# Optimization experiments

Measured on AMD Instinct MI355X. Metric: run time of the kernel, lower is better.

Reference implementation:

```python
import jax, jax.numpy as jnp
import numpy as np

TAU = 2.0        # spikingjelly LIFNode default tau
VTH = 1.0        # v_threshold
ALPHA = 2.0      # ATan surrogate alpha
NUM_HEADS = 8
N_WIN = 8
TOPK = 4


@jax.custom_vjp
def atan_heaviside(x):
    # spike = H(v - v_th), with ATan surrogate gradient
    return (x >= 0.0).astype(x.dtype)

def _ah_fwd(x):
    return atan_heaviside(x), x

def _ah_bwd(x, g):
    half_pi_alpha = np.float32(np.pi / 2.0 * ALPHA)
    return (g * (ALPHA / 2.0) / (1.0 + (half_pi_alpha * x) ** 2),)

atan_heaviside.defvjp(_ah_fwd, _ah_bwd)


def lif(x):
    """Multi-step LIF over leading time dim. decay_input=True, v_reset=0, detach_reset."""
    def step(v, xt):
        v = v + (xt - v) / TAU                      # charge
        s = atan_heaviside(v - VTH)                 # fire
        v = v * (1.0 - jax.lax.stop_gradient(s))    # hard reset (detached)
        return v, s
    _, spikes = jax.lax.scan(step, jnp.zeros_like(x[0]), x)
    return spikes


def setup_inputs() -> dict:
    key = jax.random.key(0)
    k1, k2, k3, k4, k5 = jax.random.split(key, 5)
    T, B, L, C = 4, 4, 1024, 256
    x = jax.random.normal(k1, (T, B, L, C), dtype=jnp.float32)
    w_qkv = jax.random.normal(k2, (C, 3 * C), dtype=jnp.float32) * (C ** -0.5)
    b_qkv = jax.random.normal(k3, (3 * C,), dtype=jnp.float32) * 0.02
    w_proj = jax.random.normal(k4, (C, C), dtype=jnp.float32) * (C ** -0.5)
    b_proj = jax.random.normal(k5, (C,), dtype=jnp.float32) * 0.02
    return {"x": x, "w_qkv": w_qkv, "b_qkv": b_qkv, "w_proj": w_proj, "b_proj": b_proj}


def reference(x, w_qkv, b_qkv, w_proj, b_proj):
    T, B, L, C = x.shape
    hd = C // NUM_HEADS
    win = L // N_WIN
    scale = hd ** -0.5

    # --- region-level routing (on raw input summed over time) ---
    xs = x.sum(axis=0).reshape(B, N_WIN, win, C)
    region = xs.sum(axis=2)                                  # [B, n_win, C]
    attn_r = jnp.einsum('bnc,bmc->bnm', region, region) * (C ** -0.5)
    _, idx = jax.lax.top_k(attn_r, TOPK)                     # [B, n_win, topk] int32

    # --- qkv + LIF spiking ---
    qkv = x @ w_qkv + b_qkv                                  # [T,B,L,3C]
    q, k, v = jnp.split(qkv, 3, axis=-1)
    q, k, v = lif(q), lif(k), lif(v)
    q = q.reshape(T, B, N_WIN, win, NUM_HEADS, hd)
    k = k.reshape(T, B, N_WIN, win, NUM_HEADS, hd)
    v = v.reshape(T, B, N_WIN, win, NUM_HEADS, hd)

    # --- gather routed KV windows (vectorized; topk-major concat like torch.cat) ---
    b_idx = jnp.arange(B)[:, None, None]                     # [B,1,1]
    k_g = k[:, b_idx, idx].reshape(T, B, N_WIN, TOPK * win, NUM_HEADS, hd)
    v_g = v[:, b_idx, idx].reshape(T, B, N_WIN, TOPK * win, NUM_HEADS, hd)

    # --- windowed attention over gathered keys ---
    attn = jnp.einsum('tbnqhd,tbnkhd->tbnhqk', q, k_g) * scale
    attn = jax.nn.softmax(attn, axis=-1)
    out = jnp.einsum('tbnhqk,tbnkhd->tbnqhd', attn, v_g).reshape(T, B, L, C)

    out = lif(out @ w_proj + b_proj)
    return out
```

## Files before the change

kernel.cpp:

```cpp
#include <hip/hip_runtime.h>
#include <cstdint>
#include <cstddef>

#define TT 4
#define BB 4
#define LL 1024
#define CC 256
#define HH 8
#define HD 32
#define NWIN 8
#define WIN 128
#define TOPKN 4
#define C3 768

__global__ __launch_bounds__(256) void region_kernel(const float* __restrict__ x,
                                                     float* __restrict__ region) {
    int bn = blockIdx.x;
    int b = bn >> 3, n = bn & 7;
    int c = threadIdx.x;
    float tot = 0.0f;
    for (int r = 0; r < WIN; ++r) {
        int l = n * WIN + r;
        float s = 0.0f;
        for (int t = 0; t < TT; ++t) {
            s += x[(((size_t)t * BB + b) * LL + l) * CC + c];
        }
        tot += s;
    }
    region[(size_t)bn * CC + c] = tot;
}

__global__ __launch_bounds__(64) void route_kernel(const float* __restrict__ region,
                                                   int* __restrict__ idx) {
    int b = blockIdx.x;
    __shared__ float reg[NWIN][CC];
    __shared__ float attn_r[NWIN][NWIN];
    int tid = threadIdx.x;
    for (int e = tid; e < NWIN * CC; e += 64)
        reg[e >> 8][e & 255] = region[(size_t)b * NWIN * CC + e];
    __syncthreads();
    int n = tid >> 3, m = tid & 7;
    float s = 0.0f;
    for (int c = 0; c < CC; ++c) s += reg[n][c] * reg[m][c];
    attn_r[n][m] = s * 0.0625f;
    __syncthreads();
    if (tid < NWIN) {
        float vals[NWIN];
        for (int m2 = 0; m2 < NWIN; ++m2) vals[m2] = attn_r[tid][m2];
        for (int kk = 0; kk < TOPKN; ++kk) {
            int bi = 0; float bv = vals[0];
            for (int m2 = 1; m2 < NWIN; ++m2) {
                if (vals[m2] > bv) { bv = vals[m2]; bi = m2; }
            }
            idx[(b * NWIN + tid) * TOPKN + kk] = bi;
            vals[bi] = -INFINITY;
        }
    }
}

__global__ __launch_bounds__(256, 2) void gemm_bias(const float* __restrict__ A,
                                                    const float* __restrict__ W,
                                                    const float* __restrict__ bias,
                                                    float* __restrict__ C,
                                                    int M, int N, int K) {
    const int BM = 128, BN = 128, BK = 16, TM = 8, TN = 8;
    __shared__ float As[BK][BM + 4];
    __shared__ float Bs[BK][BN];
    int tid = threadIdx.x;
    int tx = tid & 15, ty = tid >> 4;
    int bm = blockIdx.x * BM, bn = blockIdx.y * BN;
    float acc[TM][TN] = {};
    for (int k0 = 0; k0 < K; k0 += BK) {
#pragma unroll
        for (int it = 0; it < 2; ++it) {
            int i = it * 256 + tid;
            int row = i >> 2, kc = (i & 3) * 4;
            float4 v = *(const float4*)(A + (size_t)(bm + row) * K + k0 + kc);
            As[kc + 0][row] = v.x; As[kc + 1][row] = v.y;
            As[kc + 2][row] = v.z; As[kc + 3][row] = v.w;
        }
#pragma unroll
        for (int it = 0; it < 2; ++it) {
            int i = it * 256 + tid;
            int kr = i >> 5, nc = (i & 31) * 4;
            float4 v = *(const float4*)(W + (size_t)(k0 + kr) * N + bn + nc);
            *(float4*)&Bs[kr][nc] = v;
        }
        __syncthreads();
#pragma unroll
        for (int kk = 0; kk < BK; ++kk) {
            float a[TM], bb[TN];
            const float4* ap = (const float4*)&As[kk][ty * TM];
            float4 a0 = ap[0], a1 = ap[1];
            a[0]=a0.x; a[1]=a0.y; a[2]=a0.z; a[3]=a0.w;
            a[4]=a1.x; a[5]=a1.y; a[6]=a1.z; a[7]=a1.w;
            const float4* bp = (const float4*)&Bs[kk][tx * TN];
            float4 b0 = bp[0], b1 = bp[1];
            bb[0]=b0.x; bb[1]=b0.y; bb[2]=b0.z; bb[3]=b0.w;
            bb[4]=b1.x; bb[5]=b1.y; bb[6]=b1.z; bb[7]=b1.w;
#pragma unroll
            for (int i = 0; i < TM; ++i)
#pragma unroll
                for (int j = 0; j < TN; ++j)
                    acc[i][j] = fmaf(a[i], bb[j], acc[i][j]);
        }
        __syncthreads();
    }
#pragma unroll
    for (int i = 0; i < TM; ++i) {
        int row = bm + ty * TM + i;
        int col = bn + tx * TN;
        float4 o0 = make_float4(acc[i][0] + bias[col + 0], acc[i][1] + bias[col + 1],
                                acc[i][2] + bias[col + 2], acc[i][3] + bias[col + 3]);
        float4 o1 = make_float4(acc[i][4] + bias[col + 4], acc[i][5] + bias[col + 5],
                                acc[i][6] + bias[col + 6], acc[i][7] + bias[col + 7]);
        *(float4*)&C[(size_t)row * N + col]     = o0;
        *(float4*)&C[(size_t)row * N + col + 4] = o1;
    }
}

__global__ __launch_bounds__(256) void lif_kernel(const float* src, float* dst, size_t stride) {
    size_t i = ((size_t)blockIdx.x * blockDim.x + threadIdx.x) * 4;
    float v[4] = {0.f, 0.f, 0.f, 0.f};
    for (int t = 0; t < TT; ++t) {
        float4 xv4 = *(const float4*)(src + (size_t)t * stride + i);
        float xv[4] = {xv4.x, xv4.y, xv4.z, xv4.w};
        float sp[4];
#pragma unroll
        for (int j = 0; j < 4; ++j) {
            v[j] = v[j] + (xv[j] - v[j]) * 0.5f;
            bool fire = (v[j] >= 1.0f);
            sp[j] = fire ? 1.0f : 0.0f;
            v[j] = fire ? 0.0f : v[j];
        }
        *(float4*)(dst + (size_t)t * stride + i) = make_float4(sp[0], sp[1], sp[2], sp[3]);
    }
}

__global__ __launch_bounds__(256) void pack_kernel(const float* __restrict__ spk,
                                                   uint32_t* __restrict__ pk) {
    size_t g = (size_t)blockIdx.x * 256 + threadIdx.x;
    int row = (int)(g >> 9);
    int col = (int)(g & 511);
    float v = spk[(size_t)row * C3 + col];
    unsigned long long m = __ballot(v >= 0.5f);
    int lane = threadIdx.x & 63;
    if ((lane & 31) == 0)
        pk[(size_t)row * 16 + (col >> 5)] = (lane < 32) ? (uint32_t)m : (uint32_t)(m >> 32);
}

__global__ __launch_bounds__(256) void attn_sm(const uint32_t* __restrict__ pk,
                                               const int* __restrict__ idxws,
                                               float2* __restrict__ amz) {
    int bid = blockIdx.x;
    int hp = bid & 3, n = (bid >> 2) & 7, b = (bid >> 5) & 3, t = bid >> 7;
    __shared__ uint32_t kbs[2][512];
    int tid = threadIdx.x;
    int q = tid & 127, h = tid >> 7;
    int lbase = (t * BB + b) * LL;

    const int* ip = idxws + (b * NWIN + n) * TOPKN;
    int s0r = ip[0], s1r = ip[1], s2r = ip[2], s3r = ip[3];

#pragma unroll 4
    for (int e = tid; e < 1024; e += 256) {
        int hh = e >> 9, kk = e & 511;
        int w = kk >> 7;
        int sw = (w == 0) ? s0r : (w == 1) ? s1r : (w == 2) ? s2r : s3r;
        int row = sw * WIN + (kk & 127);
        kbs[hh][kk] = pk[(size_t)(lbase + row) * 16 + 8 + hp * 2 + hh];
    }
    uint32_t qw = pk[(size_t)(lbase + n * WIN + q) * 16 + hp * 2 + h];
    __syncthreads();

    const float ALPHA_SC = 0.17677669529663687f;
    const uint4* kb4 = (const uint4*)kbs[h];
    int smax = 0;
#pragma unroll 8
    for (int k4 = 0; k4 < 128; ++k4) {
        uint4 w4 = kb4[k4];
        smax = max(smax, __popc(qw & w4.x));
        smax = max(smax, __popc(qw & w4.y));
        smax = max(smax, __popc(qw & w4.z));
        smax = max(smax, __popc(qw & w4.w));
    }
    float am = __fmul_rn((float)smax, ALPHA_SC);
    float Z = 0.0f;
#pragma unroll 4
    for (int k4 = 0; k4 < 128; ++k4) {
        uint4 w4 = kb4[k4];
        Z += expf(__fsub_rn(__fmul_rn((float)__popc(qw & w4.x), ALPHA_SC), am));
        Z += expf(__fsub_rn(__fmul_rn((float)__popc(qw & w4.y), ALPHA_SC), am));
        Z += expf(__fsub_rn(__fmul_rn((float)__popc(qw & w4.z), ALPHA_SC), am));
        Z += expf(__fsub_rn(__fmul_rn((float)__popc(qw & w4.w), ALPHA_SC), am));
    }
    amz[(size_t)(lbase + n * WIN + q) * HH + hp * 2 + h] = make_float2(am, Z);
}

__global__ __launch_bounds__(128, 2) void attn_pv(const float* __restrict__ spk,
                                                  const uint32_t* __restrict__ pk,
                                                  const int* __restrict__ idxws,
                                                  const float2* __restrict__ amz,
                                                  float* __restrict__ out) {
    int bid = blockIdx.x;
    int h = bid & 1, hp = (bid >> 1) & 3, n = (bid >> 3) & 7, b = (bid >> 6) & 3, t = bid >> 8;
    __shared__ __align__(16) float Vlds[2][64][32];
    __shared__ float    ptab[33][WIN];
    __shared__ uint32_t kbs[4 * WIN];
    int tid = threadIdx.x;
    int qg = tid & 63, dh = tid >> 6;
    int lbase = (t * BB + b) * LL;

    const int* ip = idxws + (b * NWIN + n) * TOPKN;
    int sidx[TOPKN];
    sidx[0] = ip[0]; sidx[1] = ip[1]; sidx[2] = ip[2]; sidx[3] = ip[3];

#pragma unroll 4
    for (int e = tid; e < 512; e += 128) {
        int w = e >> 7;
        int sw = sidx[w];
        int row = sw * WIN + (e & 127);
        kbs[e] = pk[(size_t)(lbase + row) * 16 + 8 + hp * 2 + h];
    }
    uint32_t qw0 = pk[(size_t)(lbase + n * WIN + qg) * 16 + hp * 2 + h];
    uint32_t qw1 = pk[(size_t)(lbase + n * WIN + qg + 64) * 16 + hp * 2 + h];

    {
        float2 az = amz[(size_t)(lbase + n * WIN + tid) * HH + hp * 2 + h];
        const float ALPHA_SC = 0.17677669529663687f;
        for (int s = 0; s <= 32; ++s)
            ptab[s][tid] = expf(__fsub_rn(__fmul_rn((float)s, ALPHA_SC), az.x)) / az.y;
    }

    const float* vsrc = spk + (size_t)lbase * C3 + 512 + hp * 64 + h * 32
                        + (size_t)(tid >> 3) * C3 + (tid & 7) * 4;
    int wvoff = (tid >> 6) * 1024;

#define STAGE_HALF(hw_)                                                              \
    do {                                                                             \
        int hw = (hw_);                                                              \
        const float* src = vsrc + (size_t)sidx[hw >> 1] * (WIN * C3)                 \
                                + (size_t)(hw & 1) * 64 * C3;                        \
        char* lbasep = (char*)(&Vlds[hw & 1][0][0]) + wvoff;                         \
        _Pragma("unroll")                                                            \
        for (int it = 0; it < 4; ++it) {                                             \
            __builtin_amdgcn_global_load_lds(                                        \
                (const __attribute__((address_space(1))) void*)(src + (size_t)it * 16 * C3), \
                (__attribute__((address_space(3))) void*)(lbasep + it * 2048),       \
                16, 0, 0);                                                           \
        }                                                                            \
    } while (0)

    STAGE_HALF(0);

    float acc0[16], acc1[16];
#pragma unroll
    for (int d = 0; d < 16; ++d) { acc0[d] = 0.0f; acc1[d] = 0.0f; }

    asm volatile("s_waitcnt vmcnt(0)" ::: "memory");
    __syncthreads();

    const uint4* kb4 = (const uint4*)kbs;

#pragma unroll
    for (int hw = 0; hw < 8; ++hw) {
        if (hw < 7) STAGE_HALF(hw + 1);

        const uint4* kw4 = kb4 + hw * 16;
        const float* pr = &Vlds[hw & 1][0][dh * 16];
#pragma unroll 4
        for (int g = 0; g < 16; ++g) {
            uint4 kw = kw4[g];
#pragma unroll
            for (int j = 0; j < 4; ++j) {
                uint32_t kwj = (j == 0) ? kw.x : (j == 1) ? kw.y : (j == 2) ? kw.z : kw.w;
                float P0 = ptab[__popc(qw0 & kwj)][qg];
                float P1 = ptab[__popc(qw1 & kwj)][qg + 64];
                const float4* vp = (const float4*)(pr + j * 32);
                float4 v0 = vp[0], v1 = vp[1], v2 = vp[2], v3 = vp[3];
                acc0[ 0] = fmaf(P0, v0.x, acc0[ 0]);  acc1[ 0] = fmaf(P1, v0.x, acc1[ 0]);
                acc0[ 1] = fmaf(P0, v0.y, acc0[ 1]);  acc1[ 1] = fmaf(P1, v0.y, acc1[ 1]);
                acc0[ 2] = fmaf(P0, v0.z, acc0[ 2]);  acc1[ 2] = fmaf(P1, v0.z, acc1[ 2]);
                acc0[ 3] = fmaf(P0, v0.w, acc0[ 3]);  acc1[ 3] = fmaf(P1, v0.w, acc1[ 3]);
                acc0[ 4] = fmaf(P0, v1.x, acc0[ 4]);  acc1[ 4] = fmaf(P1, v1.x, acc1[ 4]);
                acc0[ 5] = fmaf(P0, v1.y, acc0[ 5]);  acc1[ 5] = fmaf(P1, v1.y, acc1[ 5]);
                acc0[ 6] = fmaf(P0, v1.z, acc0[ 6]);  acc1[ 6] = fmaf(P1, v1.z, acc1[ 6]);
                acc0[ 7] = fmaf(P0, v1.w, acc0[ 7]);  acc1[ 7] = fmaf(P1, v1.w, acc1[ 7]);
                acc0[ 8] = fmaf(P0, v2.x, acc0[ 8]);  acc1[ 8] = fmaf(P1, v2.x, acc1[ 8]);
                acc0[ 9] = fmaf(P0, v2.y, acc0[ 9]);  acc1[ 9] = fmaf(P1, v2.y, acc1[ 9]);
                acc0[10] = fmaf(P0, v2.z, acc0[10]);  acc1[10] = fmaf(P1, v2.z, acc1[10]);
                acc0[11] = fmaf(P0, v2.w, acc0[11]);  acc1[11] = fmaf(P1, v2.w, acc1[11]);
                acc0[12] = fmaf(P0, v3.x, acc0[12]);  acc1[12] = fmaf(P1, v3.x, acc1[12]);
                acc0[13] = fmaf(P0, v3.y, acc0[13]);  acc1[13] = fmaf(P1, v3.y, acc1[13]);
                acc0[14] = fmaf(P0, v3.z, acc0[14]);  acc1[14] = fmaf(P1, v3.z, acc1[14]);
                acc0[15] = fmaf(P0, v3.w, acc0[15]);  acc1[15] = fmaf(P1, v3.w, acc1[15]);
            }
            pr += 128;
        }

        asm volatile("s_waitcnt vmcnt(0)" ::: "memory");
        __syncthreads();
    }
#undef STAGE_HALF

    size_t ob0 = (size_t)(lbase + n * WIN + qg) * CC + (hp * 2 + h) * 32 + dh * 16;
    size_t ob1 = ob0 + (size_t)64 * CC;
#pragma unroll
    for (int d = 0; d < 16; ++d) out[ob0 + d] = acc0[d];
#pragma unroll
    for (int d = 0; d < 16; ++d) out[ob1 + d] = acc1[d];
}

extern "C" void kernel_launch(void* const* d_in, const int* in_sizes, int n_in,
                              void* d_out, int out_size, void* d_ws, size_t ws_size,
                              hipStream_t stream) {
    const float* x      = (const float*)d_in[0];
    const float* w_qkv  = (const float*)d_in[1];
    const float* b_qkv  = (const float*)d_in[2];
    const float* w_proj = (const float*)d_in[3];
    const float* b_proj = (const float*)d_in[4];
    float* ws = (float*)d_ws;

    float* qkv      = ws;
    float* attn_out = ws + 12582912;
    float* proj     = ws + 16777216;
    uint32_t* pkb   = (uint32_t*)proj;
    float* region   = ws + 20971520;
    int*   idxp     = (int*)(ws + 20979712);
    float2* amzp    = (float2*)(ws + 20979840);
    float* outp     = (float*)d_out;

    region_kernel<<<dim3(BB * NWIN), dim3(256), 0, stream>>>(x, region);
    route_kernel<<<dim3(BB), dim3(64), 0, stream>>>(region, idxp);
    gemm_bias<<<dim3(128, 6), dim3(256), 0, stream>>>(x, w_qkv, b_qkv, qkv,
                                                      TT * BB * LL, C3, CC);
    lif_kernel<<<dim3(3072), dim3(256), 0, stream>>>(qkv, qkv, (size_t)BB * LL * C3);
    pack_kernel<<<dim3(32768), dim3(256), 0, stream>>>(qkv, pkb);
    attn_sm<<<dim3(TT * BB * NWIN * 4), dim3(256), 0, stream>>>(pkb, idxp, amzp);
    attn_pv<<<dim3(TT * BB * NWIN * 4 * 2), dim3(128), 0, stream>>>(qkv, pkb, idxp, amzp, attn_out);
    gemm_bias<<<dim3(128, 2), dim3(256), 0, stream>>>(attn_out, w_proj, b_proj, proj,
                                                      TT * BB * LL, CC, CC);
    lif_kernel<<<dim3(1024), dim3(256), 0, stream>>>(proj, outp, (size_t)BB * LL * CC);
}
```

Measured before the change: 286.5 us.

## Fuse softmax stats into attention kernel, retile GEMMs, deepen V prefetch

Merges the separate softmax-statistics kernel into the PV attention kernel, so each block computes row max and normalizer from the packed spike bits in LDS and no longer round-trips them through global memory. The V staging becomes a two-deep prefetch with partial vmcnt waits so loads overlap with compute. The QKV GEMM changes its B-tile column mapping to split each thread's columns into two strided halves with padded LDS and raises its occupancy hint. The projection GEMM switches to a 64x64 tile kernel for more blocks. The fused kernel repeats the popcount max/sum work per block pair, and the extra staging adds LDS pressure.

```diff
diff --git a/kernel.cpp b/kernel.cpp
--- a/kernel.cpp
+++ b/kernel.cpp
@@ -58,18 +58,18 @@
     }
 }
 
-__global__ __launch_bounds__(256, 2) void gemm_bias(const float* __restrict__ A,
-                                                    const float* __restrict__ W,
-                                                    const float* __restrict__ bias,
-                                                    float* __restrict__ C,
-                                                    int M, int N, int K) {
-    const int BM = 128, BN = 128, BK = 16, TM = 8, TN = 8;
+__global__ __launch_bounds__(256, 3) void gemm_bias128(const float* __restrict__ A,
+                                                       const float* __restrict__ W,
+                                                       const float* __restrict__ bias,
+                                                       float* __restrict__ C,
+                                                       int M, int N, int K) {
+    const int BM = 128, BN = 128, BK = 16, TM = 8;
     __shared__ float As[BK][BM + 4];
-    __shared__ float Bs[BK][BN];
+    __shared__ float Bs[BK][136];
     int tid = threadIdx.x;
     int tx = tid & 15, ty = tid >> 4;
     int bm = blockIdx.x * BM, bn = blockIdx.y * BN;
-    float acc[TM][TN] = {};
+    float acc[TM][8] = {};
     for (int k0 = 0; k0 < K; k0 += BK) {
 #pragma unroll
         for (int it = 0; it < 2; ++it) {
@@ -89,19 +89,19 @@
         __syncthreads();
 #pragma unroll
         for (int kk = 0; kk < BK; ++kk) {
-            float a[TM], bb[TN];
+            float a[TM], bb[8];
             const float4* ap = (const float4*)&As[kk][ty * TM];
             float4 a0 = ap[0], a1 = ap[1];
             a[0]=a0.x; a[1]=a0.y; a[2]=a0.z; a[3]=a0.w;
             a[4]=a1.x; a[5]=a1.y; a[6]=a1.z; a[7]=a1.w;
-            const float4* bp = (const float4*)&Bs[kk][tx * TN];
-            float4 b0 = bp[0], b1 = bp[1];
+            float4 b0 = *(const float4*)&Bs[kk][tx * 4];
+            float4 b1 = *(const float4*)&Bs[kk][64 + tx * 4];
             bb[0]=b0.x; bb[1]=b0.y; bb[2]=b0.z; bb[3]=b0.w;
             bb[4]=b1.x; bb[5]=b1.y; bb[6]=b1.z; bb[7]=b1.w;
 #pragma unroll
             for (int i = 0; i < TM; ++i)
 #pragma unroll
-                for (int j = 0; j < TN; ++j)
+                for (int j = 0; j < 8; ++j)
                     acc[i][j] = fmaf(a[i], bb[j], acc[i][j]);
         }
         __syncthreads();
@@ -109,13 +109,63 @@
 #pragma unroll
     for (int i = 0; i < TM; ++i) {
         int row = bm + ty * TM + i;
-        int col = bn + tx * TN;
-        float4 o0 = make_float4(acc[i][0] + bias[col + 0], acc[i][1] + bias[col + 1],
-                                acc[i][2] + bias[col + 2], acc[i][3] + bias[col + 3]);
-        float4 o1 = make_float4(acc[i][4] + bias[col + 4], acc[i][5] + bias[col + 5],
-                                acc[i][6] + bias[col + 6], acc[i][7] + bias[col + 7]);
-        *(float4*)&C[(size_t)row * N + col]     = o0;
-        *(float4*)&C[(size_t)row * N + col + 4] = o1;
+        int col0 = bn + tx * 4;
+        int col1 = bn + 64 + tx * 4;
+        float4 o0 = make_float4(acc[i][0] + bias[col0 + 0], acc[i][1] + bias[col0 + 1],
+                                acc[i][2] + bias[col0 + 2], acc[i][3] + bias[col0 + 3]);
+        float4 o1 = make_float4(acc[i][4] + bias[col1 + 0], acc[i][5] + bias[col1 + 1],
+                                acc[i][6] + bias[col1 + 2], acc[i][7] + bias[col1 + 3]);
+        *(float4*)&C[(size_t)row * N + col0] = o0;
+        *(float4*)&C[(size_t)row * N + col1] = o1;
+    }
+}
+
+__global__ __launch_bounds__(256, 4) void gemm_bias64(const float* __restrict__ A,
+                                                      const float* __restrict__ W,
+                                                      const float* __restrict__ bias,
+                                                      float* __restrict__ C,
+                                                      int M, int N, int K) {
+    const int BM = 64, BN = 64, BK = 16;
+    __shared__ float As[BK][BM + 4];
+    __shared__ float Bs[BK][72];
+    int tid = threadIdx.x;
+    int tx = tid & 15, ty = tid >> 4;
+    int bm = blockIdx.x * BM, bn = blockIdx.y * BN;
+    float acc[4][4] = {};
+    for (int k0 = 0; k0 < K; k0 += BK) {
+        {
+            int row = tid >> 2, kc = (tid & 3) * 4;
+            float4 v = *(const float4*)(A + (size_t)(bm + row) * K + k0 + kc);
+            As[kc + 0][row] = v.x; As[kc + 1][row] = v.y;
+            As[kc + 2][row] = v.z; As[kc + 3][row] = v.w;
+        }
+        {
+            int kr = tid >> 4, nc = (tid & 15) * 4;
+            float4 v = *(const float4*)(W + (size_t)(k0 + kr) * N + bn + nc);
+            *(float4*)&Bs[kr][nc] = v;
+        }
+        __syncthreads();
+#pragma unroll
+        for (int kk = 0; kk < BK; ++kk) {
+            float4 av = *(const float4*)&As[kk][ty * 4];
+            float4 bv = *(const float4*)&Bs[kk][tx * 4];
+            float a[4] = {av.x, av.y, av.z, av.w};
+            float bb[4] = {bv.x, bv.y, bv.z, bv.w};
+#pragma unroll
+            for (int i = 0; i < 4; ++i)
+#pragma unroll
+                for (int j = 0; j < 4; ++j)
+                    acc[i][j] = fmaf(a[i], bb[j], acc[i][j]);
+        }
+        __syncthreads();
+    }
+#pragma unroll
+    for (int i = 0; i < 4; ++i) {
+        int row = bm + ty * 4 + i;
+        int col = bn + tx * 4;
+        float4 o = make_float4(acc[i][0] + bias[col + 0], acc[i][1] + bias[col + 1],
+                               acc[i][2] + bias[col + 2], acc[i][3] + bias[col + 3]);
+        *(float4*)&C[(size_t)row * N + col] = o;
     }
 }
 
@@ -149,64 +199,15 @@
         pk[(size_t)row * 16 + (col >> 5)] = (lane < 32) ? (uint32_t)m : (uint32_t)(m >> 32);
 }
 
-__global__ __launch_bounds__(256) void attn_sm(const uint32_t* __restrict__ pk,
-                                               const int* __restrict__ idxws,
-                                               float2* __restrict__ amz) {
-    int bid = blockIdx.x;
-    int hp = bid & 3, n = (bid >> 2) & 7, b = (bid >> 5) & 3, t = bid >> 7;
-    __shared__ uint32_t kbs[2][512];
-    int tid = threadIdx.x;
-    int q = tid & 127, h = tid >> 7;
-    int lbase = (t * BB + b) * LL;
-
-    const int* ip = idxws + (b * NWIN + n) * TOPKN;
-    int s0r = ip[0], s1r = ip[1], s2r = ip[2], s3r = ip[3];
-
-#pragma unroll 4
-    for (int e = tid; e < 1024; e += 256) {
-        int hh = e >> 9, kk = e & 511;
-        int w = kk >> 7;
-        int sw = (w == 0) ? s0r : (w == 1) ? s1r : (w == 2) ? s2r : s3r;
-        int row = sw * WIN + (kk & 127);
-        kbs[hh][kk] = pk[(size_t)(lbase + row) * 16 + 8 + hp * 2 + hh];
-    }
-    uint32_t qw = pk[(size_t)(lbase + n * WIN + q) * 16 + hp * 2 + h];
-    __syncthreads();
-
-    const float ALPHA_SC = 0.17677669529663687f;
-    const uint4* kb4 = (const uint4*)kbs[h];
-    int smax = 0;
-#pragma unroll 8
-    for (int k4 = 0; k4 < 128; ++k4) {
-        uint4 w4 = kb4[k4];
-        smax = max(smax, __popc(qw & w4.x));
-        smax = max(smax, __popc(qw & w4.y));
-        smax = max(smax, __popc(qw & w4.z));
-        smax = max(smax, __popc(qw & w4.w));
-    }
-    float am = __fmul_rn((float)smax, ALPHA_SC);
-    float Z = 0.0f;
-#pragma unroll 4
-    for (int k4 = 0; k4 < 128; ++k4) {
-        uint4 w4 = kb4[k4];
-        Z += expf(__fsub_rn(__fmul_rn((float)__popc(qw & w4.x), ALPHA_SC), am));
-        Z += expf(__fsub_rn(__fmul_rn((float)__popc(qw & w4.y), ALPHA_SC), am));
-        Z += expf(__fsub_rn(__fmul_rn((float)__popc(qw & w4.z), ALPHA_SC), am));
-        Z += expf(__fsub_rn(__fmul_rn((float)__popc(qw & w4.w), ALPHA_SC), am));
-    }
-    amz[(size_t)(lbase + n * WIN + q) * HH + hp * 2 + h] = make_float2(am, Z);
-}
-
-__global__ __launch_bounds__(128, 2) void attn_pv(const float* __restrict__ spk,
-                                                  const uint32_t* __restrict__ pk,
-                                                  const int* __restrict__ idxws,
-                                                  const float2* __restrict__ amz,
-                                                  float* __restrict__ out) {
+__global__ __launch_bounds__(128, 2) void attn_fused(const float* __restrict__ spk,
+                                                     const uint32_t* __restrict__ pk,
+                                                     const int* __restrict__ idxws,
+                                                     float* __restrict__ out) {
     int bid = blockIdx.x;
     int h = bid & 1, hp = (bid >> 1) & 3, n = (bid >> 3) & 7, b = (bid >> 6) & 3, t = bid >> 8;
     __shared__ __align__(16) float Vlds[2][64][32];
-    __shared__ float    ptab[33][WIN];
-    __shared__ uint32_t kbs[4 * WIN];
+    __shared__ float ptab[33][WIN];
+    __shared__ __align__(16) uint32_t kbs[4 * WIN];
     int tid = threadIdx.x;
     int qg = tid & 63, dh = tid >> 6;
     int lbase = (t * BB + b) * LL;
@@ -218,19 +219,13 @@
 #pragma unroll 4
     for (int e = tid; e < 512; e += 128) {
         int w = e >> 7;
-        int sw = sidx[w];
-        int row = sw * WIN + (e & 127);
+        int row = sidx[w] * WIN + (e & 127);
         kbs[e] = pk[(size_t)(lbase + row) * 16 + 8 + hp * 2 + h];
     }
     uint32_t qw0 = pk[(size_t)(lbase + n * WIN + qg) * 16 + hp * 2 + h];
     uint32_t qw1 = pk[(size_t)(lbase + n * WIN + qg + 64) * 16 + hp * 2 + h];
-
-    {
-        float2 az = amz[(size_t)(lbase + n * WIN + tid) * HH + hp * 2 + h];
-        const float ALPHA_SC = 0.17677669529663687f;
-        for (int s = 0; s <= 32; ++s)
-            ptab[s][tid] = expf(__fsub_rn(__fmul_rn((float)s, ALPHA_SC), az.x)) / az.y;
-    }
+    uint32_t qwt = pk[(size_t)(lbase + n * WIN + tid) * 16 + hp * 2 + h];
+    __syncthreads();
 
     const float* vsrc = spk + (size_t)lbase * C3 + 512 + hp * 64 + h * 32
                         + (size_t)(tid >> 3) * C3 + (tid & 7) * 4;
@@ -252,54 +247,104 @@
     } while (0)
 
     STAGE_HALF(0);
+    STAGE_HALF(1);
+
+    const float ALPHA_SC = 0.17677669529663687f;
+    const uint4* kb4 = (const uint4*)kbs;
+    int smax = 0;
+#pragma unroll 8
+    for (int k4 = 0; k4 < 128; ++k4) {
+        uint4 w4 = kb4[k4];
+        smax = max(smax, __popc(qwt & w4.x));
+        smax = max(smax, __popc(qwt & w4.y));
+        smax = max(smax, __popc(qwt & w4.z));
+        smax = max(smax, __popc(qwt & w4.w));
+    }
+    float am = __fmul_rn((float)smax, ALPHA_SC);
+    float Z = 0.0f;
+#pragma unroll 4
+    for (int k4 = 0; k4 < 128; ++k4) {
+        uint4 w4 = kb4[k4];
+        Z += expf(__fsub_rn(__fmul_rn((float)__popc(qwt & w4.x), ALPHA_SC), am));
+        Z += expf(__fsub_rn(__fmul_rn((float)__popc(qwt & w4.y), ALPHA_SC), am));
+        Z += expf(__fsub_rn(__fmul_rn((float)__popc(qwt & w4.z), ALPHA_SC), am));
+        Z += expf(__fsub_rn(__fmul_rn((float)__popc(qwt & w4.w), ALPHA_SC), am));
+    }
+    for (int s = 0; s <= 32; ++s)
+        ptab[s][tid] = expf(__fsub_rn(__fmul_rn((float)s, ALPHA_SC), am)) / Z;
 
     float acc0[16], acc1[16];
 #pragma unroll
     for (int d = 0; d < 16; ++d) { acc0[d] = 0.0f; acc1[d] = 0.0f; }
 
-    asm volatile("s_waitcnt vmcnt(0)" ::: "memory");
+    asm volatile("s_waitcnt vmcnt(4)" ::: "memory");
     __syncthreads();
 
-    const uint4* kb4 = (const uint4*)kbs;
-
 #pragma unroll
     for (int hw = 0; hw < 8; ++hw) {
-        if (hw < 7) STAGE_HALF(hw + 1);
-
         const uint4* kw4 = kb4 + hw * 16;
-        const float* pr = &Vlds[hw & 1][0][dh * 16];
-#pragma unroll 4
+        const float* vb = &Vlds[hw & 1][0][dh * 16];
+#pragma unroll 2
         for (int g = 0; g < 16; ++g) {
             uint4 kw = kw4[g];
-#pragma unroll
-            for (int j = 0; j < 4; ++j) {
-                uint32_t kwj = (j == 0) ? kw.x : (j == 1) ? kw.y : (j == 2) ? kw.z : kw.w;
-                float P0 = ptab[__popc(qw0 & kwj)][qg];
-                float P1 = ptab[__popc(qw1 & kwj)][qg + 64];
-                const float4* vp = (const float4*)(pr + j * 32);
-                float4 v0 = vp[0], v1 = vp[1], v2 = vp[2], v3 = vp[3];
-                acc0[ 0] = fmaf(P0, v0.x, acc0[ 0]);  acc1[ 0] = fmaf(P1, v0.x, acc1[ 0]);
-                acc0[ 1] = fmaf(P0, v0.y, acc0[ 1]);  acc1[ 1] = fmaf(P1, v0.y, acc1[ 1]);
-                acc0[ 2] = fmaf(P0, v0.z, acc0[ 2]);  acc1[ 2] = fmaf(P1, v0.z, acc1[ 2]);
-                acc0[ 3] = fmaf(P0, v0.w, acc0[ 3]);  acc1[ 3] = fmaf(P1, v0.w, acc1[ 3]);
-                acc0[ 4] = fmaf(P0, v1.x, acc0[ 4]);  acc1[ 4] = fmaf(P1, v1.x, acc1[ 4]);
-                acc0[ 5] = fmaf(P0, v1.y, acc0[ 5]);  acc1[ 5] = fmaf(P1, v1.y, acc1[ 5]);
-                acc0[ 6] = fmaf(P0, v1.z, acc0[ 6]);  acc1[ 6] = fmaf(P1, v1.z, acc1[ 6]);
-                acc0[ 7] = fmaf(P0, v1.w, acc0[ 7]);  acc1[ 7] = fmaf(P1, v1.w, acc1[ 7]);
-                acc0[ 8] = fmaf(P0, v2.x, acc0[ 8]);  acc1[ 8] = fmaf(P1, v2.x, acc1[ 8]);
-                acc0[ 9] = fmaf(P0, v2.y, acc0[ 9]);  acc1[ 9] = fmaf(P1, v2.y, acc1[ 9]);
-                acc0[10] = fmaf(P0, v2.z, acc0[10]);  acc1[10] = fmaf(P1, v2.z, acc1[10]);
-                acc0[11] = fmaf(P0, v2.w, acc0[11]);  acc1[11] = fmaf(P1, v2.w, acc1[11]);
-                acc0[12] = fmaf(P0, v3.x, acc0[12]);  acc1[12] = fmaf(P1, v3.x, acc1[12]);
-                acc0[13] = fmaf(P0, v3.y, acc0[13]);  acc1[13] = fmaf(P1, v3.y, acc1[13]);
-                acc0[14] = fmaf(P0, v3.z, acc0[14]);  acc1[14] = fmaf(P1, v3.z, acc1[14]);
-                acc0[15] = fmaf(P0, v3.w, acc0[15]);  acc1[15] = fmaf(P1, v3.w, acc1[15]);
+            const float* pr = vb + g * 128;
+#pragma unroll
+            for (int jp = 0; jp < 2; ++jp) {
+                uint32_t ka = (jp == 0) ? kw.x : kw.z;
+                uint32_t kb_ = (jp == 0) ? kw.y : kw.w;
+                float Pa0 = ptab[__popc(qw0 & ka)][qg];
+                float Pa1 = ptab[__popc(qw1 & ka)][qg + 64];
+                float Pb0 = ptab[__popc(qw0 & kb_)][qg];
+                float Pb1 = ptab[__popc(qw1 & kb_)][qg + 64];
+                const float4* va = (const float4*)(pr + jp * 64);
+                const float4* vbp = (const float4*)(pr + jp * 64 + 32);
+                float4 a0 = va[0], a1 = va[1], a2 = va[2], a3 = va[3];
+                float4 b0 = vbp[0], b1 = vbp[1], b2 = vbp[2], b3 = vbp[3];
+                acc0[ 0] = fmaf(Pa0, a0.x, acc0[ 0]);  acc1[ 0] = fmaf(Pa1, a0.x, acc1[ 0]);
+                acc0[ 1] = fmaf(Pa0, a0.y, acc0[ 1]);  acc1[ 1] = fmaf(Pa1, a0.y, acc1[ 1]);
+                acc0[ 2] = fmaf(Pa0, a0.z, acc0[ 2]);  acc1[ 2] = fmaf(Pa1, a0.z, acc1[ 2]);
+                acc0[ 3] = fmaf(Pa0, a0.w, acc0[ 3]);  acc1[ 3] = fmaf(Pa1, a0.w, acc1[ 3]);
+                acc0[ 4] = fmaf(Pa0, a1.x, acc0[ 4]);  acc1[ 4] = fmaf(Pa1, a1.x, acc1[ 4]);
+                acc0[ 5] = fmaf(Pa0, a1.y, acc0[ 5]);  acc1[ 5] = fmaf(Pa1, a1.y, acc1[ 5]);
+                acc0[ 6] = fmaf(Pa0, a1.z, acc0[ 6]);  acc1[ 6] = fmaf(Pa1, a1.z, acc1[ 6]);
+                acc0[ 7] = fmaf(Pa0, a1.w, acc0[ 7]);  acc1[ 7] = fmaf(Pa1, a1.w, acc1[ 7]);
+                acc0[ 8] = fmaf(Pa0, a2.x, acc0[ 8]);  acc1[ 8] = fmaf(Pa1, a2.x, acc1[ 8]);
+                acc0[ 9] = fmaf(Pa0, a2.y, acc0[ 9]);  acc1[ 9] = fmaf(Pa1, a2.y, acc1[ 9]);
+                acc0[10] = fmaf(Pa0, a2.z, acc0[10]);  acc1[10] = fmaf(Pa1, a2.z, acc1[10]);
+                acc0[11] = fmaf(Pa0, a2.w, acc0[11]);  acc1[11] = fmaf(Pa1, a2.w, acc1[11]);
+                acc0[12] = fmaf(Pa0, a3.x, acc0[12]);  acc1[12] = fmaf(Pa1, a3.x, acc1[12]);
+                acc0[13] = fmaf(Pa0, a3.y, acc0[13]);  acc1[13] = fmaf(Pa1, a3.y, acc1[13]);
+                acc0[14] = fmaf(Pa0, a3.z, acc0[14]);  acc1[14] = fmaf(Pa1, a3.z, acc1[14]);
+                acc0[15] = fmaf(Pa0, a3.w, acc0[15]);  acc1[15] = fmaf(Pa1, a3.w, acc1[15]);
+                acc0[ 0] = fmaf(Pb0, b0.x, acc0[ 0]);  acc1[ 0] = fmaf(Pb1, b0.x, acc1[ 0]);
+                acc0[ 1] = fmaf(Pb0, b0.y, acc0[ 1]);  acc1[ 1] = fmaf(Pb1, b0.y, acc1[ 1]);
+                acc0[ 2] = fmaf(Pb0, b0.z, acc0[ 2]);  acc1[ 2] = fmaf(Pb1, b0.z, acc1[ 2]);
+                acc0[ 3] = fmaf(Pb0, b0.w, acc0[ 3]);  acc1[ 3] = fmaf(Pb1, b0.w, acc1[ 3]);
+                acc0[ 4] = fmaf(Pb0, b1.x, acc0[ 4]);  acc1[ 4] = fmaf(Pb1, b1.x, acc1[ 4]);
+                acc0[ 5] = fmaf(Pb0, b1.y, acc0[ 5]);  acc1[ 5] = fmaf(Pb1, b1.y, acc1[ 5]);
+                acc0[ 6] = fmaf(Pb0, b1.z, acc0[ 6]);  acc1[ 6] = fmaf(Pb1, b1.z, acc1[ 6]);
+                acc0[ 7] = fmaf(Pb0, b1.w, acc0[ 7]);  acc1[ 7] = fmaf(Pb1, b1.w, acc1[ 7]);
+                acc0[ 8] = fmaf(Pb0, b2.x, acc0[ 8]);  acc1[ 8] = fmaf(Pb1, b2.x, acc1[ 8]);
+                acc0[ 9] = fmaf(Pb0, b2.y, acc0[ 9]);  acc1[ 9] = fmaf(Pb1, b2.y, acc1[ 9]);
+                acc0[10] = fmaf(Pb0, b2.z, acc0[10]);  acc1[10] = fmaf(Pb1, b2.z, acc1[10]);
+                acc0[11] = fmaf(Pb0, b2.w, acc0[11]);  acc1[11] = fmaf(Pb1, b2.w, acc1[11]);
+                acc0[12] = fmaf(Pb0, b3.x, acc0[12]);  acc1[12] = fmaf(Pb1, b3.x, acc1[12]);
+                acc0[13] = fmaf(Pb0, b3.y, acc0[13]);  acc1[13] = fmaf(Pb1, b3.y, acc1[13]);
+                acc0[14] = fmaf(Pb0, b3.z, acc0[14]);  acc1[14] = fmaf(Pb1, b3.z, acc1[14]);
+                acc0[15] = fmaf(Pb0, b3.w, acc0[15]);  acc1[15] = fmaf(Pb1, b3.w, acc1[15]);
             }
-            pr += 128;
-        }
-
-        asm volatile("s_waitcnt vmcnt(0)" ::: "memory");
-        __syncthreads();
+        }
+
+        if (hw < 7) {
+            __syncthreads();
+            if (hw < 6) {
+                STAGE_HALF(hw + 2);
+                asm volatile("s_waitcnt vmcnt(4)" ::: "memory");
+            } else {
+                asm volatile("s_waitcnt vmcnt(0)" ::: "memory");
+            }
+            __syncthreads();
+        }
     }
 #undef STAGE_HALF
 
@@ -327,18 +372,16 @@
     uint32_t* pkb   = (uint32_t*)proj;
     float* region   = ws + 20971520;
     int*   idxp     = (int*)(ws + 20979712);
-    float2* amzp    = (float2*)(ws + 20979840);
     float* outp     = (float*)d_out;
 
     region_kernel<<<dim3(BB * NWIN), dim3(256), 0, stream>>>(x, region);
     route_kernel<<<dim3(BB), dim3(64), 0, stream>>>(region, idxp);
-    gemm_bias<<<dim3(128, 6), dim3(256), 0, stream>>>(x, w_qkv, b_qkv, qkv,
-                                                      TT * BB * LL, C3, CC);
+    gemm_bias128<<<dim3(128, 6), dim3(256), 0, stream>>>(x, w_qkv, b_qkv, qkv,
+                                                         TT * BB * LL, C3, CC);
     lif_kernel<<<dim3(3072), dim3(256), 0, stream>>>(qkv, qkv, (size_t)BB * LL * C3);
     pack_kernel<<<dim3(32768), dim3(256), 0, stream>>>(qkv, pkb);
-    attn_sm<<<dim3(TT * BB * NWIN * 4), dim3(256), 0, stream>>>(pkb, idxp, amzp);
-    attn_pv<<<dim3(TT * BB * NWIN * 4 * 2), dim3(128), 0, stream>>>(qkv, pkb, idxp, amzp, attn_out);
-    gemm_bias<<<dim3(128, 2), dim3(256), 0, stream>>>(attn_out, w_proj, b_proj, proj,
-                                                      TT * BB * LL, CC, CC);
+    attn_fused<<<dim3(TT * BB * NWIN * 4 * 2), dim3(128), 0, stream>>>(qkv, pkb, idxp, attn_out);
+    gemm_bias64<<<dim3(256, 4), dim3(256), 0, stream>>>(attn_out, w_proj, b_proj, proj,
+                                                        TT * BB * LL, CC, CC);
     lif_kernel<<<dim3(1024), dim3(256), 0, stream>>>(proj, outp, (size_t)BB * LL * CC);
 }
```

Result: faster. 274.5 us (-4.2%).
